# Performance work log

Measured on AMD Instinct MI355X. Metric: run time of the kernel, lower is better.

## Reference

```python
import jax, jax.numpy as jnp
import numpy as np

D = 256   # model dim
M = 64    # num mechanisms
B = 4
S = 8192


def setup_inputs() -> dict:
    key = jax.random.key(0)
    ks = jax.random.split(key, 16)
    n = jax.random.normal
    inp = {
        "x": n(ks[0], (B, S, D), jnp.float32),
        "context": n(ks[1], (B, S, D), jnp.float32),
        # stacked per-mechanism params (m, out, in) etc.
        "Wm": n(ks[2], (M, D, D), jnp.float32) * (1.0 / np.sqrt(D)),
        "bm": n(ks[3], (M, D), jnp.float32) * 0.02,
        "cm": n(ks[4], (M, D), jnp.float32),           # characteristics (1,1,dim) per node
        "um": n(ks[5], (M, D), jnp.float32) * (1.0 / np.sqrt(D)),  # timing_gate weight
        "vm": n(ks[6], (M,), jnp.float32) * 0.02,       # timing_gate bias
        # selector: Linear(d, 2d) -> GELU -> Linear(2d, m)
        "W1": n(ks[7], (2 * D, D), jnp.float32) * (1.0 / np.sqrt(D)),
        "b1": n(ks[8], (2 * D,), jnp.float32) * 0.02,
        "W2": n(ks[9], (M, 2 * D), jnp.float32) * (1.0 / np.sqrt(2 * D)),
        "b2": n(ks[10], (M,), jnp.float32) * 0.02,
        # integrate: Linear(2d, d)
        "Wi": n(ks[11], (D, 2 * D), jnp.float32) * (1.0 / np.sqrt(2 * D)),
        "bi": n(ks[12], (D,), jnp.float32) * 0.02,
    }
    return inp


def reference(x, context, Wm, bm, cm, um, vm, W1, b1, W2, b2, Wi, bi):
    # selector: softmax over mechanisms (b, s, m)
    h = jax.nn.gelu(jnp.einsum('bsd,ed->bse', context, W1) + b1, approximate=False)
    scores = jax.nn.softmax(jnp.einsum('bse,me->bsm', h, W2) + b2, axis=-1)

    # per-mechanism sigmoid timing gate (b, s, m)
    gate = jax.nn.sigmoid(jnp.einsum('bsd,md->bsm', x, um) + vm)

    # combined weight a[b,s,m] = softmax_score * gate; then
    # selected = sum_m a * (x @ Wm.T + bm + cm)  -- contracted without
    # materializing the (b, s, m, d) stack the torch loop builds.
    a = scores * gate                               # (b, s, m)
    selected = jnp.einsum('bsm,bse,mde->bsd', a, x, Wm) \
             + jnp.einsum('bsm,md->bsd', a, bm + cm)

    # integrate(concat([x, selected]))
    cat = jnp.concatenate([x, selected], axis=-1)   # (b, s, 2d)
    integrated = jnp.einsum('bse,de->bsd', cat, Wi) + bi
    return integrated
```

## Files before the change

### kernel.cpp

```cpp
#include <hip/hip_runtime.h>
#include <cstdint>
#include <cstddef>


typedef _Float16 f16;
typedef f16 f16x8 __attribute__((ext_vector_type(8)));
typedef float f32x4 __attribute__((ext_vector_type(4)));
typedef float f32x16 __attribute__((ext_vector_type(16)));

#define DEV __device__ __forceinline__

DEV uint32_t swz128(uint32_t b) { return b ^ (((b >> 7) & 7u) << 4); }

DEV void gload_lds16(const void* g, void* l) {
  __builtin_amdgcn_global_load_lds(
      (const __attribute__((address_space(1))) unsigned int*)g,
      (__attribute__((address_space(3))) unsigned int*)l, 16, 0, 0);
}

DEV f16x8 cvt8(float4 u0, float4 u1) {
  f16x8 v = {(f16)u0.x, (f16)u0.y, (f16)u0.z, (f16)u0.w,
             (f16)u1.x, (f16)u1.y, (f16)u1.z, (f16)u1.w};
  return v;
}

__global__ void prep_b_kernel(const float* __restrict__ S, f16* __restrict__ dst,
                              int K, int BN, int total) {
  int t = blockIdx.x * 256 + threadIdx.x;
  if (t >= total) return;
  int gpc = BN * 8;
  int g = t % gpc;
  int c = (t / gpc) % (K / 64);
  int cb = t / (gpc * (K / 64));
  int ks = g / (BN * 4);
  int rem = g % (BN * 4);
  int col = rem >> 2;
  int kg = rem & 3;
  int J = cb * BN + col;
  int k = c * 64 + ks * 32 + kg * 8;
  const float* s = S + (size_t)J * K + k;
  float4 u0 = *(const float4*)s;
  float4 u1 = *(const float4*)(s + 4);
  f16* chunk = dst + (size_t)(cb * (K / 64) + c) * (BN * 64);
  *(f16x8*)((char*)chunk + swz128((uint32_t)g * 16)) = cvt8(u0, u1);
}

__global__ void prep_wcat_kernel(const float* __restrict__ Wm,
                                 const float* __restrict__ bm,
                                 const float* __restrict__ cm,
                                 f16* __restrict__ dst) {
  int t = blockIdx.x * 256 + threadIdx.x;
  if (t >= 4 * 257 * 512) return;
  int g = t & 511;
  int gc = t >> 9;
  int c = gc % 257;
  int cb = gc / 257;
  int kstep = g >> 7;
  int khalf = (g >> 6) & 1;
  int col = cb * 64 + (g & 63);
  int k0 = kstep * 16 + khalf * 8;
  f16x8 v;
  if (c < 256) {
    int m = c & 63;
    int e0 = (c >> 6) * 64 + k0;
    const float* s = Wm + ((size_t)m * 256 + col) * 256 + e0;
    float4 u0 = *(const float4*)s;
    float4 u1 = *(const float4*)(s + 4);
    v = cvt8(u0, u1);
  } else {
#pragma unroll
    for (int j = 0; j < 8; ++j) {
      int k = k0 + j;
      v[j] = (f16)(bm[k * 256 + col] + cm[k * 256 + col]);
    }
  }
  *(f16x8*)(dst + ((size_t)(cb * 260 + c)) * 4096 + (size_t)g * 8) = v;
}

template <int BN, int NCHUNK, int A0C, int EPI>
__global__ __launch_bounds__(BN == 256 ? 512 : 256, 2)
void gemm_tpl(const float* __restrict__ A0, int lda0,
              const f16* __restrict__ A1, int lda1,
              const f16* __restrict__ Bt,
              const float* __restrict__ bias,
              float* __restrict__ outF, f16* __restrict__ outH, int ldo) {
  constexpr int WAVES = (BN == 256) ? 8 : 4;
  constexpr int THREADS = WAVES * 64;
  constexpr int WC = (BN == 256) ? 4 : 1;
  constexpr int WR = WAVES / WC;
  constexpr int RT = 128 / (WR * 16);
  constexpr int CT = (BN / WC) / 16;

  __shared__ alignas(16) f16 sA[2][128 * 64];
  __shared__ alignas(16) f16 sB[2][BN * 64];

  const int tid = threadIdx.x;
  const int lane = tid & 63;
  const int wid = tid >> 6;
  const int wr = wid / WC, wc = wid % WC;
  const int rb = blockIdx.x, cb = blockIdx.y;

  auto stageB = [&](int c, int buf) {
    const char* src = (const char*)(Bt + (size_t)(cb * NCHUNK + c) * (BN * 64));
#pragma unroll
    for (int it = 0; it < (BN * 64 * 2) / (THREADS * 16); ++it) {
      int off = (it * THREADS + tid) * 16;
      gload_lds16(src + off, (char*)&sB[buf][0] + off);
    }
  };
  auto stageA = [&](int c, int buf) {
#pragma unroll
    for (int it = 0; it < 1024 / THREADS; ++it) {
      int gg = it * THREADS + tid;
      int row = gg >> 3, eg = gg & 7;
      size_t rowG = (size_t)rb * 128 + row;
      f16x8 v;
      if (A0C > 0 && c < A0C) {
        const float* s = A0 + rowG * lda0 + c * 64 + eg * 8;
        float4 u0 = *(const float4*)s;
        float4 u1 = *(const float4*)(s + 4);
        v = cvt8(u0, u1);
      } else {
        v = *(const f16x8*)(A1 + rowG * lda1 + (c - A0C) * 64 + eg * 8);
      }
      *(f16x8*)((char*)&sA[buf][0] + swz128((uint32_t)(row * 128 + eg * 16))) = v;
    }
  };

  f32x4 acc[RT][CT];
#pragma unroll
  for (int i = 0; i < RT; ++i)
#pragma unroll
    for (int j = 0; j < CT; ++j) acc[i][j] = (f32x4){0.f, 0.f, 0.f, 0.f};

  stageB(0, 0);
  stageA(0, 0);
  __syncthreads();

  for (int c = 0; c < NCHUNK; ++c) {
    int cur = c & 1;
    if (c + 1 < NCHUNK) {
      stageB(c + 1, cur ^ 1);
      stageA(c + 1, cur ^ 1);
    }
#pragma unroll
    for (int ks = 0; ks < 2; ++ks) {
      f16x8 af[RT], bf[CT];
#pragma unroll
      for (int rt = 0; rt < RT; ++rt) {
        int row = wr * (RT * 16) + rt * 16 + (lane & 15);
        af[rt] = *(const f16x8*)((const char*)&sA[cur][0] +
                                 swz128((uint32_t)(row * 128 + ks * 64 + (lane >> 4) * 16)));
      }
#pragma unroll
      for (int ct = 0; ct < CT; ++ct) {
        int col = wc * (CT * 16) + ct * 16 + (lane & 15);
        bf[ct] = *(const f16x8*)((const char*)&sB[cur][0] +
                                 swz128((uint32_t)(((ks * BN + col) * 4 + (lane >> 4)) * 16)));
      }
#pragma unroll
      for (int rt = 0; rt < RT; ++rt)
#pragma unroll
        for (int ct = 0; ct < CT; ++ct)
          acc[rt][ct] = __builtin_amdgcn_mfma_f32_16x16x32_f16(af[rt], bf[ct], acc[rt][ct], 0, 0, 0);
    }
    __syncthreads();
  }

#pragma unroll
  for (int rt = 0; rt < RT; ++rt)
#pragma unroll
    for (int ct = 0; ct < CT; ++ct)
#pragma unroll
      for (int i = 0; i < 4; ++i) {
        size_t row = (size_t)rb * 128 + wr * (RT * 16) + rt * 16 + (lane >> 4) * 4 + i;
        int colG = cb * BN + wc * (CT * 16) + ct * 16 + (lane & 15);
        float v = acc[rt][ct][i];
        if constexpr (EPI == 0) {
          if (bias) v += bias[colG];
          outF[row * ldo + colG] = v;
        } else {
          v += bias[colG];
          float ge = 0.5f * v * (1.0f + erff(v * 0.70710678118f));
          outH[row * ldo + colG] = (f16)ge;
        }
      }
}

__global__ void selector_finish(const float* __restrict__ logits,
                                const float* __restrict__ glog,
                                const float* __restrict__ b2,
                                const float* __restrict__ vm,
                                f16* __restrict__ a16s) {
  int n = blockIdx.x * 4 + (threadIdx.x >> 6);
  int m = threadIdx.x & 63;
  float l = logits[(size_t)n * 64 + m] + b2[m];
  float mx = l;
#pragma unroll
  for (int o = 32; o; o >>= 1) mx = fmaxf(mx, __shfl_xor(mx, o));
  float p = expf(l - mx);
  float s = p;
#pragma unroll
  for (int o = 32; o; o >>= 1) s += __shfl_xor(s, o);
  float g = glog[(size_t)n * 64 + m] + vm[m];
  float gate = 1.0f / (1.0f + expf(-g));
  int rb = n >> 8, row = n & 255, gg = m >> 3, j = m & 7;
  a16s[(size_t)rb * 16384 + gg * 2048 + row * 8 + j] = (f16)(p / s * gate);
}

__global__ __launch_bounds__(256, 2)
void big_gemm(const float* __restrict__ x, const f16* __restrict__ a16s,
              const f16* __restrict__ Wcat, f16* __restrict__ sel) {
  __shared__ alignas(16) f16 sB[3][128 * 64];
  __shared__ alignas(16) f16 sAa[8 * 256 * 8];

  const int tid = threadIdx.x;
  const int lane = tid & 63;
  const int wid = tid >> 6;
  const int l31 = lane & 31;
  const int khalf = lane >> 5;
  const int bid = blockIdx.x;
  const int xcd = bid & 7;
  const int cb = xcd >> 1;
  const int rb = (xcd & 1) * 64 + (bid >> 3);
  const f16* Wb = Wcat + (size_t)cb * 260 * 4096;
  const int rbase = wid * 64 + l31;

  char* const sBbase = (char*)&sB[0][0];

  auto stagePair = [&](int p, int slotIdx) {
    const char* src = (const char*)Wb + (size_t)p * 16384;
    char* dst = sBbase + slotIdx * 16384;
#pragma unroll
    for (int it = 0; it < 4; ++it) {
      int off = (it * 256 + tid) * 16;
      gload_lds16(src + off, dst + off);
    }
  };

  {
    const char* aSrc = (const char*)(a16s + (size_t)rb * 16384);
#pragma unroll
    for (int it = 0; it < 8; ++it) {
      int off = (it * 256 + tid) * 16;
      gload_lds16(aSrc + off, (char*)sAa + off);
    }
  }
  stagePair(0, 0);
  stagePair(1, 1);
  asm volatile("s_waitcnt vmcnt(4)" ::: "memory");
  __builtin_amdgcn_s_barrier();
  __builtin_amdgcn_sched_barrier(0);

  f32x16 acc[2][2];
#pragma unroll
  for (int i = 0; i < 2; ++i)
#pragma unroll
    for (int j = 0; j < 2; ++j)
#pragma unroll
      for (int r = 0; r < 16; ++r) acc[i][j][r] = 0.f;

  f16x8 xv[2][4];
  auto loadXV = [&](int er) {
#pragma unroll
    for (int rt = 0; rt < 2; ++rt)
#pragma unroll
      for (int ks = 0; ks < 4; ++ks) {
        const float* s = x + ((size_t)rb * 256 + rbase + rt * 32) * 256
                           + er * 64 + ks * 16 + khalf * 8;
        float4 u0 = *(const float4*)s;
        float4 u1 = *(const float4*)(s + 4);
        xv[rt][ks] = cvt8(u0, u1);
      }
  };

  const int bOff = khalf * 1024 + l31 * 16;

  for (int q8g = 0; q8g < 32; ++q8g) {
    const int q8 = q8g * 8;
    if ((q8 & 63) == 0) loadXV(q8 >> 6);
    f16x8 as_cur[2];
    {
      int g = (q8 & 63) >> 3;
#pragma unroll
      for (int rt = 0; rt < 2; ++rt)
        as_cur[rt] = *(const f16x8*)((const char*)sAa + ((g * 256) + rbase + rt * 32) * 16);
    }
#pragma unroll
    for (int p = 0; p < 4; ++p) {
      const int pj = (q8 >> 1) + p;
      f16x8 af0[2][4];
#pragma unroll
      for (int rt = 0; rt < 2; ++rt)
#pragma unroll
        for (int ks = 0; ks < 4; ++ks)
          af0[rt][ks] = xv[rt][ks] * as_cur[rt][2 * p + 0];
      asm volatile("s_waitcnt vmcnt(4)" ::: "memory");
      __builtin_amdgcn_s_barrier();
      __builtin_amdgcn_sched_barrier(0);
      stagePair(pj + 2, (pj + 2) % 3);
      const char* base = sBbase + (pj % 3) * 16384 + bOff;
      f16x8 bfA[8], bfB[8];
#pragma unroll
      for (int ks = 0; ks < 4; ++ks)
#pragma unroll
        for (int ct = 0; ct < 2; ++ct) {
          bfA[ks * 2 + ct] = *(const f16x8*)(base + ks * 2048 + ct * 512);
          bfB[ks * 2 + ct] = *(const f16x8*)(base + 8192 + ks * 2048 + ct * 512);
        }
      __builtin_amdgcn_s_setprio(1);
#pragma unroll
      for (int ks = 0; ks < 4; ++ks)
#pragma unroll
        for (int rt = 0; rt < 2; ++rt)
#pragma unroll
          for (int ct = 0; ct < 2; ++ct)
            acc[rt][ct] = __builtin_amdgcn_mfma_f32_32x32x16_f16(
                af0[rt][ks], bfA[ks * 2 + ct], acc[rt][ct], 0, 0, 0);
      __builtin_amdgcn_s_setprio(0);
      f16x8 af1[2][4];
#pragma unroll
      for (int rt = 0; rt < 2; ++rt)
#pragma unroll
        for (int ks = 0; ks < 4; ++ks)
          af1[rt][ks] = xv[rt][ks] * as_cur[rt][2 * p + 1];
      __builtin_amdgcn_s_setprio(1);
#pragma unroll
      for (int ks = 0; ks < 4; ++ks)
#pragma unroll
        for (int rt = 0; rt < 2; ++rt)
#pragma unroll
          for (int ct = 0; ct < 2; ++ct)
            acc[rt][ct] = __builtin_amdgcn_mfma_f32_32x32x16_f16(
                af1[rt][ks], bfB[ks * 2 + ct], acc[rt][ct], 0, 0, 0);
      __builtin_amdgcn_s_setprio(0);
    }
  }

  asm volatile("s_waitcnt vmcnt(4)" ::: "memory");
  __builtin_amdgcn_s_barrier();
#pragma unroll
  for (int ks = 0; ks < 4; ++ks)
#pragma unroll
    for (int rt = 0; rt < 2; ++rt) {
      int g = ks * 2 + khalf;
      f16x8 af = *(const f16x8*)((const char*)sAa + ((g * 256) + rbase + rt * 32) * 16);
#pragma unroll
      for (int ct = 0; ct < 2; ++ct) {
        f16x8 bf = *(const f16x8*)(sBbase + 2 * 16384 + bOff + ks * 2048 + ct * 512);
        acc[rt][ct] = __builtin_amdgcn_mfma_f32_32x32x16_f16(af, bf, acc[rt][ct], 0, 0, 0);
      }
    }

#pragma unroll
  for (int rt = 0; rt < 2; ++rt)
#pragma unroll
    for (int ct = 0; ct < 2; ++ct)
#pragma unroll
      for (int r = 0; r < 16; ++r) {
        int rowin = (r & 3) + 8 * (r >> 2) + 4 * khalf;
        size_t row = (size_t)rb * 256 + wid * 64 + rt * 32 + rowin;
        int col = cb * 64 + ct * 32 + l31;
        sel[row * 256 + col] = (f16)acc[rt][ct][r];
      }
}

extern "C" void kernel_launch(void* const* d_in, const int* in_sizes, int n_in,
                              void* d_out, int out_size, void* d_ws, size_t ws_size,
                              hipStream_t stream) {
  (void)in_sizes; (void)n_in; (void)out_size;
  const float* x   = (const float*)d_in[0];
  const float* ctx = (const float*)d_in[1];
  const float* Wm  = (const float*)d_in[2];
  const float* bm  = (const float*)d_in[3];
  const float* cm  = (const float*)d_in[4];
  const float* um  = (const float*)d_in[5];
  const float* vm  = (const float*)d_in[6];
  const float* W1  = (const float*)d_in[7];
  const float* b1  = (const float*)d_in[8];
  const float* W2  = (const float*)d_in[9];
  const float* b2  = (const float*)d_in[10];
  const float* Wi  = (const float*)d_in[11];
  const float* bi  = (const float*)d_in[12];
  float* out = (float*)d_out;

  char* ws = (char*)d_ws;
  size_t off = 0;
  f16* Wcat = (f16*)(ws + off); off += (size_t)4 * 260 * 4096 * 2;
  f16* W1t  = (f16*)(ws + off); off += (size_t)512 * 256 * 2;
  f16* W2t  = (f16*)(ws + off); off += (size_t)64 * 512 * 2;
  f16* umt  = (f16*)(ws + off); off += (size_t)64 * 256 * 2;
  f16* Wit  = (f16*)(ws + off); off += (size_t)256 * 512 * 2;
  f16* h16  = (f16*)(ws + off); off += (size_t)32768 * 512 * 2;
  float* logits = (float*)(ws + off); off += (size_t)32768 * 64 * 4;
  float* glog   = (float*)(ws + off); off += (size_t)32768 * 64 * 4;
  f16* a16s  = (f16*)(ws + off); off += (size_t)32768 * 64 * 2;
  f16* sel16 = (f16*)(ws + off); off += (size_t)32768 * 256 * 2;
  if (ws_size < off) return;

  prep_wcat_kernel<<<dim3(2056), dim3(256), 0, stream>>>(Wm, bm, cm, Wcat);
  prep_b_kernel<<<dim3(16384 / 256), dim3(256), 0, stream>>>(W1, W1t, 256, 256, 16384);
  prep_b_kernel<<<dim3(4096 / 256),  dim3(256), 0, stream>>>(W2, W2t, 512, 64, 4096);
  prep_b_kernel<<<dim3(2048 / 256),  dim3(256), 0, stream>>>(um, umt, 256, 64, 2048);
  prep_b_kernel<<<dim3(16384 / 256), dim3(256), 0, stream>>>(Wi, Wit, 512, 256, 16384);

  gemm_tpl<256, 4, 4, 1><<<dim3(256, 2), dim3(512), 0, stream>>>(
      ctx, 256, nullptr, 0, W1t, b1, nullptr, h16, 512);
  gemm_tpl<64, 4, 4, 0><<<dim3(256, 1), dim3(256), 0, stream>>>(
      x, 256, nullptr, 0, umt, nullptr, glog, nullptr, 64);
  gemm_tpl<64, 8, 0, 0><<<dim3(256, 1), dim3(256), 0, stream>>>(
      nullptr, 0, h16, 512, W2t, nullptr, logits, nullptr, 64);
  selector_finish<<<dim3(32768 / 4), dim3(256), 0, stream>>>(logits, glog, b2, vm, a16s);

  big_gemm<<<dim3(512), dim3(256), 0, stream>>>(x, a16s, Wcat, sel16);

  gemm_tpl<256, 8, 4, 0><<<dim3(256, 1), dim3(512), 0, stream>>>(
      x, 256, sel16, 256, Wit, bi, out, nullptr, 256);
}
```

Baseline: 351.0 us.

## Load weight fragments directly from global into registers, dropping LDS staging and barriers

The big GEMM no longer stages the per-mechanism weight tiles through a triple-buffered LDS ring with block barriers. Each wave now loads its B fragments straight from global memory into two register buffers, prefetching two mechanisms ahead in a ping-pong. This removes the per-step barriers and the LDS traffic, and frees 48KB of shared memory. In exchange it raises register pressure and has every wave issue redundant global/L2 loads of the same weight data.

```diff
diff --git a/kernel.cpp b/kernel.cpp
--- a/kernel.cpp
+++ b/kernel.cpp
@@ -211,7 +211,6 @@
 __global__ __launch_bounds__(256, 2)
 void big_gemm(const float* __restrict__ x, const f16* __restrict__ a16s,
               const f16* __restrict__ Wcat, f16* __restrict__ sel) {
-  __shared__ alignas(16) f16 sB[3][128 * 64];
   __shared__ alignas(16) f16 sAa[8 * 256 * 8];
 
   const int tid = threadIdx.x;
@@ -223,20 +222,8 @@
   const int xcd = bid & 7;
   const int cb = xcd >> 1;
   const int rb = (xcd & 1) * 64 + (bid >> 3);
-  const f16* Wb = Wcat + (size_t)cb * 260 * 4096;
+  const char* Wb = (const char*)(Wcat + (size_t)cb * 260 * 4096);
   const int rbase = wid * 64 + l31;
-
-  char* const sBbase = (char*)&sB[0][0];
-
-  auto stagePair = [&](int p, int slotIdx) {
-    const char* src = (const char*)Wb + (size_t)p * 16384;
-    char* dst = sBbase + slotIdx * 16384;
-#pragma unroll
-    for (int it = 0; it < 4; ++it) {
-      int off = (it * 256 + tid) * 16;
-      gload_lds16(src + off, dst + off);
-    }
-  };
 
   {
     const char* aSrc = (const char*)(a16s + (size_t)rb * 16384);
@@ -246,11 +233,10 @@
       gload_lds16(aSrc + off, (char*)sAa + off);
     }
   }
-  stagePair(0, 0);
-  stagePair(1, 1);
-  asm volatile("s_waitcnt vmcnt(4)" ::: "memory");
+  asm volatile("s_waitcnt vmcnt(0)" ::: "memory");
   __builtin_amdgcn_s_barrier();
-  __builtin_amdgcn_sched_barrier(0);
+
+  const int bOff = khalf * 1024 + l31 * 16;
 
   f32x16 acc[2][2];
 #pragma unroll
@@ -273,12 +259,20 @@
         xv[rt][ks] = cvt8(u0, u1);
       }
   };
-
-  const int bOff = khalf * 1024 + l31 * 16;
+  loadXV(0);
+
+  f16x8 bf0[8], bf1[8];
+#pragma unroll
+  for (int ks = 0; ks < 4; ++ks)
+#pragma unroll
+    for (int ct = 0; ct < 2; ++ct) {
+      bf0[ks * 2 + ct] = *(const f16x8*)(Wb + 0 * 8192 + bOff + ks * 2048 + ct * 512);
+      bf1[ks * 2 + ct] = *(const f16x8*)(Wb + 1 * 8192 + bOff + ks * 2048 + ct * 512);
+    }
 
   for (int q8g = 0; q8g < 32; ++q8g) {
     const int q8 = q8g * 8;
-    if ((q8 & 63) == 0) loadXV(q8 >> 6);
+    if ((q8 & 63) == 0 && q8 > 0) loadXV(q8 >> 6);
     f16x8 as_cur[2];
     {
       int g = (q8 & 63) >> 3;
@@ -287,58 +281,51 @@
         as_cur[rt] = *(const f16x8*)((const char*)sAa + ((g * 256) + rbase + rt * 32) * 16);
     }
 #pragma unroll
-    for (int p = 0; p < 4; ++p) {
-      const int pj = (q8 >> 1) + p;
-      f16x8 af0[2][4];
+    for (int u = 0; u < 8; ++u) {
+      const int q = q8 + u;
+      f16x8 af[2][4];
 #pragma unroll
       for (int rt = 0; rt < 2; ++rt)
 #pragma unroll
         for (int ks = 0; ks < 4; ++ks)
-          af0[rt][ks] = xv[rt][ks] * as_cur[rt][2 * p + 0];
-      asm volatile("s_waitcnt vmcnt(4)" ::: "memory");
-      __builtin_amdgcn_s_barrier();
-      __builtin_amdgcn_sched_barrier(0);
-      stagePair(pj + 2, (pj + 2) % 3);
-      const char* base = sBbase + (pj % 3) * 16384 + bOff;
-      f16x8 bfA[8], bfB[8];
-#pragma unroll
-      for (int ks = 0; ks < 4; ++ks)
-#pragma unroll
-        for (int ct = 0; ct < 2; ++ct) {
-          bfA[ks * 2 + ct] = *(const f16x8*)(base + ks * 2048 + ct * 512);
-          bfB[ks * 2 + ct] = *(const f16x8*)(base + 8192 + ks * 2048 + ct * 512);
-        }
-      __builtin_amdgcn_s_setprio(1);
-#pragma unroll
-      for (int ks = 0; ks < 4; ++ks)
-#pragma unroll
-        for (int rt = 0; rt < 2; ++rt)
+          af[rt][ks] = xv[rt][ks] * as_cur[rt][u];
+      const char* nsrc = Wb + (size_t)(q + 2) * 8192 + bOff;
+      if ((u & 1) == 0) {
+        __builtin_amdgcn_s_setprio(1);
+#pragma unroll
+        for (int ks = 0; ks < 4; ++ks)
+#pragma unroll
+          for (int rt = 0; rt < 2; ++rt)
+#pragma unroll
+            for (int ct = 0; ct < 2; ++ct)
+              acc[rt][ct] = __builtin_amdgcn_mfma_f32_32x32x16_f16(
+                  af[rt][ks], bf0[ks * 2 + ct], acc[rt][ct], 0, 0, 0);
+        __builtin_amdgcn_s_setprio(0);
+#pragma unroll
+        for (int ks = 0; ks < 4; ++ks)
 #pragma unroll
           for (int ct = 0; ct < 2; ++ct)
-            acc[rt][ct] = __builtin_amdgcn_mfma_f32_32x32x16_f16(
-                af0[rt][ks], bfA[ks * 2 + ct], acc[rt][ct], 0, 0, 0);
-      __builtin_amdgcn_s_setprio(0);
-      f16x8 af1[2][4];
-#pragma unroll
-      for (int rt = 0; rt < 2; ++rt)
+            bf0[ks * 2 + ct] = *(const f16x8*)(nsrc + ks * 2048 + ct * 512);
+      } else {
+        __builtin_amdgcn_s_setprio(1);
 #pragma unroll
         for (int ks = 0; ks < 4; ++ks)
-          af1[rt][ks] = xv[rt][ks] * as_cur[rt][2 * p + 1];
-      __builtin_amdgcn_s_setprio(1);
-#pragma unroll
-      for (int ks = 0; ks < 4; ++ks)
-#pragma unroll
-        for (int rt = 0; rt < 2; ++rt)
+#pragma unroll
+          for (int rt = 0; rt < 2; ++rt)
+#pragma unroll
+            for (int ct = 0; ct < 2; ++ct)
+              acc[rt][ct] = __builtin_amdgcn_mfma_f32_32x32x16_f16(
+                  af[rt][ks], bf1[ks * 2 + ct], acc[rt][ct], 0, 0, 0);
+        __builtin_amdgcn_s_setprio(0);
+#pragma unroll
+        for (int ks = 0; ks < 4; ++ks)
 #pragma unroll
           for (int ct = 0; ct < 2; ++ct)
-            acc[rt][ct] = __builtin_amdgcn_mfma_f32_32x32x16_f16(
-                af1[rt][ks], bfB[ks * 2 + ct], acc[rt][ct], 0, 0, 0);
-      __builtin_amdgcn_s_setprio(0);
+            bf1[ks * 2 + ct] = *(const f16x8*)(nsrc + ks * 2048 + ct * 512);
+      }
     }
   }
 
-  asm volatile("s_waitcnt vmcnt(4)" ::: "memory");
-  __builtin_amdgcn_s_barrier();
 #pragma unroll
   for (int ks = 0; ks < 4; ++ks)
 #pragma unroll
@@ -346,10 +333,9 @@
       int g = ks * 2 + khalf;
       f16x8 af = *(const f16x8*)((const char*)sAa + ((g * 256) + rbase + rt * 32) * 16);
 #pragma unroll
-      for (int ct = 0; ct < 2; ++ct) {
-        f16x8 bf = *(const f16x8*)(sBbase + 2 * 16384 + bOff + ks * 2048 + ct * 512);
-        acc[rt][ct] = __builtin_amdgcn_mfma_f32_32x32x16_f16(af, bf, acc[rt][ct], 0, 0, 0);
-      }
+      for (int ct = 0; ct < 2; ++ct)
+        acc[rt][ct] = __builtin_amdgcn_mfma_f32_32x32x16_f16(
+            af, bf0[ks * 2 + ct], acc[rt][ct], 0, 0, 0);
     }
 
 #pragma unroll
```

After: 376.2 us. +7.2%, slower.
